# Kernel optimization log

Hardware: AMD Instinct MI355X
Metric: run time of the kernel (lower is better)

The kernel has to match this reference:

```python
import jax, jax.numpy as jnp
import numpy as np

B, L, V, A = 4096, 64, 50000, 1000
E, H, G, F2 = 32, 32, 256, 512


def _xavier(k, shape):
    fan_out, fan_in = shape
    a = np.sqrt(6.0 / (fan_in + fan_out)).astype(np.float32)
    return jax.random.uniform(k, shape, jnp.float32, -a, a)


def setup_inputs() -> dict:
    key = jax.random.key(0)
    ks = jax.random.split(key, 32)
    inp = {}
    inp["q"] = jax.random.randint(ks[0], (B, L), 0, V)
    for i in range(8):
        inp[f"sf{i}"] = jax.random.randint(ks[1 + i], (B, L), 0, V)
    inp["emb"] = _xavier(ks[9], (V, E))
    # torch LSTM weight layout: [4H, in] with gate order i,f,g,o; biases init to 0
    inp["q_Wih"] = _xavier(ks[10], (4 * H, E))
    inp["q_Whh"] = _xavier(ks[11], (4 * H, H))
    inp["q_b"] = jnp.zeros((4 * H,), jnp.float32)
    inp["sf_Wih"] = _xavier(ks[12], (4 * H, E))
    inp["sf_Whh"] = _xavier(ks[13], (4 * H, H))
    inp["sf_b"] = jnp.zeros((4 * H,), jnp.float32)
    inp["g1_W"] = _xavier(ks[14], (G, 2 * H + 1)); inp["g1_b"] = jnp.zeros((G,), jnp.float32)
    inp["g2_W"] = _xavier(ks[15], (G, G)); inp["g2_b"] = jnp.zeros((G,), jnp.float32)
    inp["g3_W"] = _xavier(ks[16], (G, G)); inp["g3_b"] = jnp.zeros((G,), jnp.float32)
    inp["g4_W"] = _xavier(ks[17], (G, G)); inp["g4_b"] = jnp.zeros((G,), jnp.float32)
    inp["f1_W"] = _xavier(ks[18], (G, G)); inp["f1_b"] = jnp.zeros((G,), jnp.float32)
    inp["f2_W"] = _xavier(ks[19], (F2, G)); inp["f2_b"] = jnp.zeros((F2,), jnp.float32)
    inp["f3_W"] = _xavier(ks[20], (A, F2)); inp["f3_b"] = jnp.zeros((A,), jnp.float32)
    return inp


def _lstm_last(x, Wih, Whh, b):
    """x: [L, N, E] -> final hidden state [N, H]. Torch gate order i,f,g,o."""
    n = x.shape[1]
    h_dim = Whh.shape[1]
    def step(carry, xt):
        h, c = carry
        gates = xt @ Wih.T + h @ Whh.T + b  # [N, 4H]
        i, f, g, o = jnp.split(gates, 4, axis=-1)
        c = jax.nn.sigmoid(f) * c + jax.nn.sigmoid(i) * jnp.tanh(g)
        h = jax.nn.sigmoid(o) * jnp.tanh(c)
        return (h, c), None
    init = (jnp.zeros((n, h_dim), x.dtype), jnp.zeros((n, h_dim), x.dtype))
    (h, _), _ = jax.lax.scan(step, init, x)
    return h


def _lin(x, W, b):
    return x @ W.T + b


def reference(q, sf0, sf1, sf2, sf3, sf4, sf5, sf6, sf7,
              emb, q_Wih, q_Whh, q_b, sf_Wih, sf_Whh, sf_b,
              g1_W, g1_b, g2_W, g2_b, g3_W, g3_b, g4_W, g4_b,
              f1_W, f1_b, f2_W, f2_b, f3_W, f3_b):
    # dropout in eval mode (identity)
    b, l = q.shape
    qe = emb[q].transpose(1, 0, 2)  # [L, B, E]
    hq = _lstm_last(qe, q_Wih, q_Whh, q_b)  # [B, H]

    sf = jnp.stack([sf0, sf1, sf2, sf3, sf4, sf5, sf6, sf7])  # [8, B, L]
    sfe = emb[sf]  # [8, B, L, E]
    sfe = sfe.transpose(2, 0, 1, 3).reshape(l, 8 * b, emb.shape[1])  # one fused LSTM over 8*B
    hs = _lstm_last(sfe, sf_Wih, sf_Whh, sf_b).reshape(8, b, -1)  # [8, B, H]

    pos = jnp.broadcast_to(jnp.arange(8, dtype=hs.dtype)[:, None, None], (8, b, 1))
    x = jnp.concatenate([hs, jnp.broadcast_to(hq, (8, b, hq.shape[-1])), pos], axis=-1)  # [8, B, 65]
    x = jax.nn.relu(_lin(x, g1_W, g1_b))
    x = jax.nn.relu(_lin(x, g2_W, g2_b))
    x = jax.nn.relu(_lin(x, g3_W, g3_b))
    x = jax.nn.relu(_lin(x, g4_W, g4_b))
    g_o = x.sum(axis=0)  # [B, 256] segment-sum over the 8 relations

    x = jax.nn.relu(_lin(g_o, f1_W, f1_b))
    x = jax.nn.relu(_lin(x, f2_W, f2_b))
    return _lin(x, f3_W, f3_b)  # [B, A]
```

## Files before the change

### kernel.cpp

```cpp
#include <hip/hip_runtime.h>
#include <stdint.h>
#include <stddef.h>

typedef __fp16 f16;
typedef __attribute__((ext_vector_type(8))) __fp16 half8;
typedef __attribute__((ext_vector_type(4))) __fp16 half4;
typedef __attribute__((ext_vector_type(4))) float f32x4;

static __device__ __forceinline__ f32x4 mfma16(half8 a, half8 b, f32x4 c) {
    return __builtin_amdgcn_mfma_f32_16x16x32_f16(a, b, c, 0, 0, 0);
}
static __device__ __forceinline__ float fexp2(float x) { float r; asm("v_exp_f32 %0, %1" : "=v"(r) : "v"(x)); return r; }
static __device__ __forceinline__ float frcp(float x)  { float r; asm("v_rcp_f32 %0, %1" : "=v"(r) : "v"(x)); return r; }

static constexpr float L2E  = 1.4426950408889634f;
static constexpr float L2E2 = 2.8853900817779268f;

static constexpr int LDA = 264;
static constexpr int LDF2 = 520;

static constexpr size_t OFF_EMB   = 0;
static constexpr size_t OFF_WQIH  = 3200000;
static constexpr size_t OFF_WQHH  = OFF_WQIH + 8192;
static constexpr size_t OFF_WSIH  = OFF_WQHH + 8192;
static constexpr size_t OFF_WSHH  = OFF_WSIH + 8192;
static constexpr size_t OFF_BQ    = OFF_WSHH + 8192;
static constexpr size_t OFF_BS    = OFF_BQ + 512;
static constexpr size_t OFF_G1WP  = OFF_BS + 512;
static constexpr size_t OFF_BIAS8 = OFF_G1WP + 32768;
static constexpr size_t OFF_G2W   = OFF_BIAS8 + 8192;
static constexpr size_t OFF_G3W   = OFF_G2W + 131072;
static constexpr size_t OFF_G4W   = OFF_G3W + 131072;
static constexpr size_t OFF_F1W   = OFF_G4W + 131072;
static constexpr size_t OFF_F2W   = OFF_F1W + 131072;
static constexpr size_t OFF_F3W   = OFF_F2W + 262144;
static constexpr size_t OFF_HS    = OFF_F3W + 1024000;
static constexpr size_t OFF_HQ    = OFF_HS + 2097152;
static constexpr size_t OFF_ACT2  = OFF_HQ + 262144;
static constexpr size_t WS_NEED   = OFF_ACT2 + 16777216;

struct CvtJobs { const float* src[7]; f16* dst[7]; int n[7]; };

__global__ __launch_bounds__(256) void cvt_prep(
    CvtJobs j,
    const float* __restrict__ g1W, const float* __restrict__ g1b,
    f16* __restrict__ wp, float* __restrict__ bias8,
    const float* __restrict__ qWih, const float* __restrict__ qWhh, const float* __restrict__ qb,
    const float* __restrict__ sWih, const float* __restrict__ sWhh, const float* __restrict__ sb,
    f16* __restrict__ wqih, f16* __restrict__ wqhh, float* __restrict__ bq,
    f16* __restrict__ wsih, f16* __restrict__ wshh, float* __restrict__ bs)
{
    int t = threadIdx.x;
    if (blockIdx.y < 7) {
        int jb = blockIdx.y;
        int i = (blockIdx.x * 256 + t) * 8;
        if (i >= j.n[jb]) return;
        const float* s = j.src[jb] + i;
        f32x4 a = *(const f32x4*)s;
        f32x4 b = *(const f32x4*)(s + 4);
        half8 o;
        o[0]=(f16)a[0]; o[1]=(f16)a[1]; o[2]=(f16)a[2]; o[3]=(f16)a[3];
        o[4]=(f16)b[0]; o[5]=(f16)b[1]; o[6]=(f16)b[2]; o[7]=(f16)b[3];
        *(half8*)(j.dst[jb] + i) = o;
        return;
    }
    if (blockIdx.x == 0) {
        int col = t;
        for (int k = 0; k < 64; k++) wp[col * 64 + k] = (f16)g1W[col * 65 + k];
        float wpos = g1W[col * 65 + 64];
        float b = g1b[col];
        for (int i = 0; i < 8; i++) bias8[i * 256 + col] = b + (float)i * wpos;
    } else if (blockIdx.x == 1) {
        for (int i = t; i < 4096; i += 256) {
            int row = i >> 5;
            float s = (row < 64 || row >= 96) ? -L2E : L2E2;
            wqih[i] = (f16)(qWih[i] * s);
            wqhh[i] = (f16)(qWhh[i] * s);
            wsih[i] = (f16)(sWih[i] * s);
            wshh[i] = (f16)(sWhh[i] * s);
        }
        if (t < 128) {
            float s = (t < 64 || t >= 96) ? -L2E : L2E2;
            bq[t] = qb[t] * s;
            bs[t] = sb[t] * s;
        }
    }
}

struct SfPtrs { const int* p[8]; };

__global__ __launch_bounds__(64) void lstm_kernel(
    SfPtrs sf, const int* __restrict__ qtok, const f16* __restrict__ emb_h,
    const f16* __restrict__ wih_sf, const f16* __restrict__ whh_sf, const float* __restrict__ b_sf,
    const f16* __restrict__ wih_q,  const f16* __restrict__ whh_q,  const float* __restrict__ b_q,
    f16* __restrict__ hs_out, f16* __restrict__ hq_out)
{
    __shared__ __align__(16) char hb0[16 * 80];
    __shared__ __align__(16) char hb1[16 * 80];
    int lane = threadIdx.x;
    int c15 = lane & 15, kq = lane >> 4;
    int sbase = blockIdx.x * 32;
    bool isq = sbase >= 32768;
    const f16* wih = isq ? wih_q : wih_sf;
    const f16* whh = isq ? whh_q : whh_sf;
    const float* bvec = isq ? b_q : b_sf;

    half8 wi[8], wh[8];
    f32x4 bc[8];
    #pragma unroll
    for (int n = 0; n < 8; n++) {
        wi[n] = *(const half8*)(wih + (n * 16 + c15) * 32 + kq * 8);
        wh[n] = *(const half8*)(whh + (n * 16 + c15) * 32 + kq * 8);
        bc[n] = *(const f32x4*)(bvec + n * 16 + kq * 4);
    }
    int sg0 = sbase + c15, sg1 = sbase + 16 + c15;
    const int* tp0; const int* tp1;
    if (isq) { tp0 = qtok + (sg0 - 32768) * 64; tp1 = qtok + (sg1 - 32768) * 64; }
    else     { tp0 = sf.p[sg0 >> 12] + (sg0 & 4095) * 64;
               tp1 = sf.p[sg1 >> 12] + (sg1 & 4095) * 64; }

    f32x4 zro = {0.f, 0.f, 0.f, 0.f};
    *(f32x4*)(hb0 + lane * 16) = zro;
    *(f32x4*)(hb1 + lane * 16) = zro;
    if (lane < 16) { *(f32x4*)(hb0 + 1024 + lane * 16) = zro;
                     *(f32x4*)(hb1 + 1024 + lane * 16) = zro; }

    float cst0[2][4] = {}, cst1[2][4] = {};
    const char* hrd0 = hb0 + c15 * 80 + kq * 16;
    const char* hrd1 = hb1 + c15 * 80 + kq * 16;

    half8 xf0 = *(const half8*)(emb_h + (size_t)tp0[0] * 32 + kq * 8);
    half8 xf1 = *(const half8*)(emb_h + (size_t)tp1[0] * 32 + kq * 8);

    #pragma unroll 1
    for (int t = 0; t < 64; t++) {
        half8 hf0 = *(const half8*)hrd0;
        half8 hf1 = *(const half8*)hrd1;
        f32x4 a0[8], a1[8];
        #pragma unroll
        for (int n = 0; n < 8; n++) a0[n] = mfma16(wi[n], xf0, bc[n]);
        #pragma unroll
        for (int n = 0; n < 8; n++) a1[n] = mfma16(wi[n], xf1, bc[n]);
        #pragma unroll
        for (int n = 0; n < 8; n++) a0[n] = mfma16(wh[n], hf0, a0[n]);
        #pragma unroll
        for (int n = 0; n < 8; n++) a1[n] = mfma16(wh[n], hf1, a1[n]);
        if (t < 63) {
            xf0 = *(const half8*)(emb_h + (size_t)tp0[t + 1] * 32 + kq * 8);
            xf1 = *(const half8*)(emb_h + (size_t)tp1[t + 1] * 32 + kq * 8);
        }
        #pragma unroll
        for (int jh = 0; jh < 2; jh++) {
            half4 hp;
            #pragma unroll
            for (int r = 0; r < 4; r++) {
                float ei = fexp2(a0[0 + jh][r]);
                float ef = fexp2(a0[2 + jh][r]);
                float eg = fexp2(a0[4 + jh][r]);
                float eo = fexp2(a0[6 + jh][r]);
                float t1 = 1.f + ei, t2 = 1.f + ef, t5 = 1.f + eo;
                float eg1 = eg + 1.f, egm = eg - 1.f;
                float num = fmaf(egm, t2, cst0[jh][r] * t1 * eg1);
                float cn  = num * frcp((t2 * t1) * eg1);
                cst0[jh][r] = cn;
                float ec  = fexp2(cn * L2E2);
                hp[r] = (f16)((ec - 1.f) * frcp((ec + 1.f) * t5));
            }
            *(half4*)(hb0 + c15 * 80 + jh * 32 + kq * 8) = hp;
        }
        #pragma unroll
        for (int jh = 0; jh < 2; jh++) {
            half4 hp;
            #pragma unroll
            for (int r = 0; r < 4; r++) {
                float ei = fexp2(a1[0 + jh][r]);
                float ef = fexp2(a1[2 + jh][r]);
                float eg = fexp2(a1[4 + jh][r]);
                float eo = fexp2(a1[6 + jh][r]);
                float t1 = 1.f + ei, t2 = 1.f + ef, t5 = 1.f + eo;
                float eg1 = eg + 1.f, egm = eg - 1.f;
                float num = fmaf(egm, t2, cst1[jh][r] * t1 * eg1);
                float cn  = num * frcp((t2 * t1) * eg1);
                cst1[jh][r] = cn;
                float ec  = fexp2(cn * L2E2);
                hp[r] = (f16)((ec - 1.f) * frcp((ec + 1.f) * t5));
            }
            *(half4*)(hb1 + c15 * 80 + jh * 32 + kq * 8) = hp;
        }
    }
    half8 hv0 = *(const half8*)hrd0;
    half8 hv1 = *(const half8*)hrd1;
    if (isq) {
        *(half8*)(hq_out + (size_t)(sg0 - 32768) * 32 + kq * 8) = hv0;
        *(half8*)(hq_out + (size_t)(sg1 - 32768) * 32 + kq * 8) = hv1;
    } else {
        *(half8*)(hs_out + (size_t)sg0 * 32 + kq * 8) = hv0;
        *(half8*)(hs_out + (size_t)sg1 * 32 + kq * 8) = hv1;
    }
}

template<bool TOGLOBAL>
static __device__ __forceinline__ void layer256(
    const f16 (* __restrict__ src)[LDA], f16 (* __restrict__ dst)[LDA],
    const f16* __restrict__ W, const float* __restrict__ bias,
    f16* __restrict__ gout, int m0, int wm, int wn, int c15, int kq)
{
    f32x4 acc[2][4];
    #pragma unroll
    for (int a = 0; a < 2; a++)
        #pragma unroll
        for (int b = 0; b < 4; b++) acc[a][b] = (f32x4){0.f, 0.f, 0.f, 0.f};
    #pragma unroll
    for (int k0 = 0; k0 < 8; k0++) {
        half8 av[2], bv[4];
        #pragma unroll
        for (int fm = 0; fm < 2; fm++) av[fm] = *(const half8*)(&src[wm * 32 + fm * 16 + c15][k0 * 32 + kq * 8]);
        #pragma unroll
        for (int fn = 0; fn < 4; fn++) bv[fn] = *(const half8*)(W + (size_t)(wn * 64 + fn * 16 + c15) * 256 + k0 * 32 + kq * 8);
        #pragma unroll
        for (int fm = 0; fm < 2; fm++)
            #pragma unroll
            for (int fn = 0; fn < 4; fn++) acc[fm][fn] = mfma16(av[fm], bv[fn], acc[fm][fn]);
    }
    #pragma unroll
    for (int fn = 0; fn < 4; fn++) {
        int col = wn * 64 + fn * 16 + c15;
        float bb = bias[col];
        #pragma unroll
        for (int fm = 0; fm < 2; fm++)
            #pragma unroll
            for (int r = 0; r < 4; r++) {
                float v = fmaxf(acc[fm][fn][r] + bb, 0.f);
                int row = wm * 32 + fm * 16 + kq * 4 + r;
                if (TOGLOBAL) gout[(size_t)(m0 + row) * 256 + col] = (f16)v;
                else          dst[row][col] = (f16)v;
            }
    }
}

__global__ __launch_bounds__(512) void gemm_g1234(
    const f16* __restrict__ hs, const f16* __restrict__ hq,
    const f16* __restrict__ g1wp, const float* __restrict__ bias8,
    const f16* __restrict__ g2w, const float* __restrict__ g2b,
    const f16* __restrict__ g3w, const float* __restrict__ g3b,
    const f16* __restrict__ g4w, const float* __restrict__ g4b,
    f16* __restrict__ act2)
{
    __shared__ __align__(16) f16 actA[64][LDA];
    __shared__ __align__(16) f16 actB[64][LDA];
    const int wv = threadIdx.x >> 6, lane = threadIdx.x & 63;
    const int c15 = lane & 15, kq = lane >> 4;
    const int wm = wv >> 2, wn = wv & 3;
    const int m0 = blockIdx.x * 64;
    const float* brow = bias8 + ((m0 >> 12) << 8);

    {
        f32x4 acc[2][4];
        #pragma unroll
        for (int a = 0; a < 2; a++)
            #pragma unroll
            for (int b = 0; b < 4; b++) acc[a][b] = (f32x4){0.f, 0.f, 0.f, 0.f};
        half8 av[2], bv[4];
        #pragma unroll
        for (int fm = 0; fm < 2; fm++) av[fm] = *(const half8*)(hs + (size_t)(m0 + wm * 32 + fm * 16 + c15) * 32 + kq * 8);
        #pragma unroll
        for (int fn = 0; fn < 4; fn++) bv[fn] = *(const half8*)(g1wp + (size_t)(wn * 64 + fn * 16 + c15) * 64 + kq * 8);
        #pragma unroll
        for (int fm = 0; fm < 2; fm++)
            #pragma unroll
            for (int fn = 0; fn < 4; fn++) acc[fm][fn] = mfma16(av[fm], bv[fn], acc[fm][fn]);
        #pragma unroll
        for (int fm = 0; fm < 2; fm++) av[fm] = *(const half8*)(hq + (size_t)((m0 + wm * 32 + fm * 16 + c15) & 4095) * 32 + kq * 8);
        #pragma unroll
        for (int fn = 0; fn < 4; fn++) bv[fn] = *(const half8*)(g1wp + (size_t)(wn * 64 + fn * 16 + c15) * 64 + 32 + kq * 8);
        #pragma unroll
        for (int fm = 0; fm < 2; fm++)
            #pragma unroll
            for (int fn = 0; fn < 4; fn++) acc[fm][fn] = mfma16(av[fm], bv[fn], acc[fm][fn]);
        #pragma unroll
        for (int fn = 0; fn < 4; fn++) {
            int col = wn * 64 + fn * 16 + c15;
            float bb = brow[col];
            #pragma unroll
            for (int fm = 0; fm < 2; fm++)
                #pragma unroll
                for (int r = 0; r < 4; r++)
                    actA[wm * 32 + fm * 16 + kq * 4 + r][col] = (f16)fmaxf(acc[fm][fn][r] + bb, 0.f);
        }
    }
    __syncthreads();
    layer256<false>(actA, actB, g2w, g2b, nullptr, m0, wm, wn, c15, kq);
    __syncthreads();
    layer256<false>(actB, actA, g3w, g3b, nullptr, m0, wm, wn, c15, kq);
    __syncthreads();
    layer256<true>(actA, actB, g4w, g4b, act2, m0, wm, wn, c15, kq);
}

__global__ __launch_bounds__(512) void f123s_kernel(
    const f16* __restrict__ act2,
    const f16* __restrict__ f1w, const float* __restrict__ f1b,
    const f16* __restrict__ f2w, const float* __restrict__ f2b,
    const f16* __restrict__ f3w, const float* __restrict__ f3b,
    float* __restrict__ out)
{
    __shared__ __align__(16) f16 smbuf[16][LDA];
    __shared__ __align__(16) f16 f1buf[16][LDA];
    __shared__ __align__(16) f16 f2buf[16][LDF2];
    const int b0 = blockIdx.x * 16;

    {
        int r = threadIdx.x >> 5, cb = (threadIdx.x & 31) * 8;
        float s[8] = {};
        #pragma unroll
        for (int i = 0; i < 8; i++) {
            half8 v = *(const half8*)(act2 + ((size_t)(i * 4096 + b0 + r)) * 256 + cb);
            #pragma unroll
            for (int q = 0; q < 8; q++) s[q] += (float)v[q];
        }
        half8 o;
        #pragma unroll
        for (int q = 0; q < 8; q++) o[q] = (f16)s[q];
        *(half8*)(&smbuf[r][cb]) = o;
    }
    __syncthreads();
    const int wv = threadIdx.x >> 6, lane = threadIdx.x & 63;
    const int c15 = lane & 15, kq = lane >> 4;

    {
        f32x4 acc[2];
        acc[0] = (f32x4){0.f, 0.f, 0.f, 0.f}; acc[1] = acc[0];
        #pragma unroll
        for (int k0 = 0; k0 < 8; k0++) {
            half8 a = *(const half8*)(&smbuf[c15][k0 * 32 + kq * 8]);
            #pragma unroll
            for (int fn = 0; fn < 2; fn++) {
                half8 bv = *(const half8*)(f1w + (size_t)(wv * 32 + fn * 16 + c15) * 256 + k0 * 32 + kq * 8);
                acc[fn] = mfma16(a, bv, acc[fn]);
            }
        }
        #pragma unroll
        for (int fn = 0; fn < 2; fn++) {
            int col = wv * 32 + fn * 16 + c15;
            float bb = f1b[col];
            #pragma unroll
            for (int r = 0; r < 4; r++)
                f1buf[kq * 4 + r][col] = (f16)fmaxf(acc[fn][r] + bb, 0.f);
        }
    }
    __syncthreads();
    {
        f32x4 acc[4];
        #pragma unroll
        for (int b = 0; b < 4; b++) acc[b] = (f32x4){0.f, 0.f, 0.f, 0.f};
        #pragma unroll
        for (int k0 = 0; k0 < 8; k0++) {
            half8 a = *(const half8*)(&f1buf[c15][k0 * 32 + kq * 8]);
            #pragma unroll
            for (int fn = 0; fn < 4; fn++) {
                half8 bv = *(const half8*)(f2w + (size_t)(wv * 64 + fn * 16 + c15) * 256 + k0 * 32 + kq * 8);
                acc[fn] = mfma16(a, bv, acc[fn]);
            }
        }
        #pragma unroll
        for (int fn = 0; fn < 4; fn++) {
            int col = wv * 64 + fn * 16 + c15;
            float bb = f2b[col];
            #pragma unroll
            for (int r = 0; r < 4; r++)
                f2buf[kq * 4 + r][col] = (f16)fmaxf(acc[fn][r] + bb, 0.f);
        }
    }
    __syncthreads();
    {
        f32x4 acc[8];
        #pragma unroll
        for (int b = 0; b < 8; b++) acc[b] = (f32x4){0.f, 0.f, 0.f, 0.f};
        #pragma unroll
        for (int k0 = 0; k0 < 16; k0++) {
            half8 a = *(const half8*)(&f2buf[c15][k0 * 32 + kq * 8]);
            #pragma unroll
            for (int fn = 0; fn < 8; fn++) {
                int col = wv * 128 + fn * 16 + c15;
                int cl = col < 1000 ? col : 999;
                half8 bv = *(const half8*)(f3w + (size_t)cl * 512 + k0 * 32 + kq * 8);
                acc[fn] = mfma16(a, bv, acc[fn]);
            }
        }
        #pragma unroll
        for (int fn = 0; fn < 8; fn++) {
            int col = wv * 128 + fn * 16 + c15;
            if (col < 1000) {
                float bb = f3b[col];
                #pragma unroll
                for (int r = 0; r < 4; r++)
                    out[(size_t)(b0 + kq * 4 + r) * 1000 + col] = acc[fn][r] + bb;
            }
        }
    }
}

extern "C" void kernel_launch(void* const* d_in, const int* in_sizes, int n_in,
                              void* d_out, int out_size, void* d_ws, size_t ws_size,
                              hipStream_t stream)
{
    if (ws_size < WS_NEED) return;
    const int* q_tok = (const int*)d_in[0];
    SfPtrs sf;
    for (int i = 0; i < 8; i++) sf.p[i] = (const int*)d_in[1 + i];
    const float* emb_f = (const float*)d_in[9];
    const float* qWih = (const float*)d_in[10];
    const float* qWhh = (const float*)d_in[11];
    const float* q_b  = (const float*)d_in[12];
    const float* sWih = (const float*)d_in[13];
    const float* sWhh = (const float*)d_in[14];
    const float* s_b  = (const float*)d_in[15];
    const float* g1W  = (const float*)d_in[16];
    const float* g1b  = (const float*)d_in[17];
    const float* g2W  = (const float*)d_in[18];
    const float* g2b  = (const float*)d_in[19];
    const float* g3W  = (const float*)d_in[20];
    const float* g3b  = (const float*)d_in[21];
    const float* g4W  = (const float*)d_in[22];
    const float* g4b  = (const float*)d_in[23];
    const float* f1W  = (const float*)d_in[24];
    const float* f1b  = (const float*)d_in[25];
    const float* f2W  = (const float*)d_in[26];
    const float* f2b  = (const float*)d_in[27];
    const float* f3W  = (const float*)d_in[28];
    const float* f3b  = (const float*)d_in[29];

    char* ws = (char*)d_ws;
    f16* emb_h = (f16*)(ws + OFF_EMB);
    f16* wqih  = (f16*)(ws + OFF_WQIH);
    f16* wqhh  = (f16*)(ws + OFF_WQHH);
    f16* wsih  = (f16*)(ws + OFF_WSIH);
    f16* wshh  = (f16*)(ws + OFF_WSHH);
    float* bq  = (float*)(ws + OFF_BQ);
    float* bs  = (float*)(ws + OFF_BS);
    f16* g1wp  = (f16*)(ws + OFF_G1WP);
    float* bias8 = (float*)(ws + OFF_BIAS8);
    f16* g2w = (f16*)(ws + OFF_G2W);
    f16* g3w = (f16*)(ws + OFF_G3W);
    f16* g4w = (f16*)(ws + OFF_G4W);
    f16* f1w = (f16*)(ws + OFF_F1W);
    f16* f2w = (f16*)(ws + OFF_F2W);
    f16* f3w = (f16*)(ws + OFF_F3W);
    f16* hs  = (f16*)(ws + OFF_HS);
    f16* hq  = (f16*)(ws + OFF_HQ);
    f16* act2 = (f16*)(ws + OFF_ACT2);

    CvtJobs cj;
    const float* srcs[7] = {emb_f, g2W, g3W, g4W, f1W, f2W, f3W};
    f16* dsts[7]         = {emb_h, g2w, g3w, g4w, f1w, f2w, f3w};
    int ns[7] = {1600000, 65536, 65536, 65536, 65536, 131072, 512000};
    for (int i = 0; i < 7; i++) { cj.src[i] = srcs[i]; cj.dst[i] = dsts[i]; cj.n[i] = ns[i]; }

    cvt_prep<<<dim3(782, 8), 256, 0, stream>>>(cj, g1W, g1b, g1wp, bias8,
                                               qWih, qWhh, q_b, sWih, sWhh, s_b,
                                               wqih, wqhh, bq, wsih, wshh, bs);
    lstm_kernel<<<1152, 64, 0, stream>>>(sf, q_tok, emb_h, wsih, wshh, bs, wqih, wqhh, bq, hs, hq);
    gemm_g1234<<<512, 512, 0, stream>>>(hs, hq, g1wp, bias8, g2w, g2b, g3w, g3b, g4w, g4b, act2);
    f123s_kernel<<<256, 512, 0, stream>>>(act2, f1w, f1b, f2w, f2b, f3w, f3b, (float*)d_out);
}
```

Before: 394.1 us.

## Exchange LSTM hidden state via ds_bpermute and halve sequences per wave

The LSTM kernel now handles 16 sequences per 64-lane block instead of 32, doubling the grid. It drops the shared-memory round trip for the hidden state and instead rebuilds the MFMA B-operand fragment directly from the gate outputs using eight ds_bpermute lane shuffles per step. The aim is to shorten the serial per-step dependency chain (LDS write, then read) and to raise occupancy with more, lighter waves. In exchange, each wave no longer interleaves two independent recurrences to hide MFMA and transcendental latency.

```diff
diff --git a/kernel.cpp b/kernel.cpp
--- a/kernel.cpp
+++ b/kernel.cpp
@@ -6,6 +6,9 @@
 typedef __attribute__((ext_vector_type(8))) __fp16 half8;
 typedef __attribute__((ext_vector_type(4))) __fp16 half4;
 typedef __attribute__((ext_vector_type(4))) float f32x4;
+typedef unsigned int u32;
+typedef __attribute__((ext_vector_type(2))) u32 u32x2;
+typedef __attribute__((ext_vector_type(4))) u32 u32x4;
 
 static __device__ __forceinline__ f32x4 mfma16(half8 a, half8 b, f32x4 c) {
     return __builtin_amdgcn_mfma_f32_16x16x32_f16(a, b, c, 0, 0, 0);
@@ -95,11 +98,9 @@
     const f16* __restrict__ wih_q,  const f16* __restrict__ whh_q,  const float* __restrict__ b_q,
     f16* __restrict__ hs_out, f16* __restrict__ hq_out)
 {
-    __shared__ __align__(16) char hb0[16 * 80];
-    __shared__ __align__(16) char hb1[16 * 80];
     int lane = threadIdx.x;
     int c15 = lane & 15, kq = lane >> 4;
-    int sbase = blockIdx.x * 32;
+    int sbase = blockIdx.x * 16;
     bool isq = sbase >= 32768;
     const f16* wih = isq ? wih_q : wih_sf;
     const f16* whh = isq ? whh_q : whh_sf;
@@ -113,90 +114,69 @@
         wh[n] = *(const half8*)(whh + (n * 16 + c15) * 32 + kq * 8);
         bc[n] = *(const f32x4*)(bvec + n * 16 + kq * 4);
     }
-    int sg0 = sbase + c15, sg1 = sbase + 16 + c15;
-    const int* tp0; const int* tp1;
-    if (isq) { tp0 = qtok + (sg0 - 32768) * 64; tp1 = qtok + (sg1 - 32768) * 64; }
-    else     { tp0 = sf.p[sg0 >> 12] + (sg0 & 4095) * 64;
-               tp1 = sf.p[sg1 >> 12] + (sg1 & 4095) * 64; }
-
-    f32x4 zro = {0.f, 0.f, 0.f, 0.f};
-    *(f32x4*)(hb0 + lane * 16) = zro;
-    *(f32x4*)(hb1 + lane * 16) = zro;
-    if (lane < 16) { *(f32x4*)(hb0 + 1024 + lane * 16) = zro;
-                     *(f32x4*)(hb1 + 1024 + lane * 16) = zro; }
-
-    float cst0[2][4] = {}, cst1[2][4] = {};
-    const char* hrd0 = hb0 + c15 * 80 + kq * 16;
-    const char* hrd1 = hb1 + c15 * 80 + kq * 16;
-
-    half8 xf0 = *(const half8*)(emb_h + (size_t)tp0[0] * 32 + kq * 8);
-    half8 xf1 = *(const half8*)(emb_h + (size_t)tp1[0] * 32 + kq * 8);
+    int sg = sbase + c15;
+    const int* tp;
+    if (isq) tp = qtok + (sg - 32768) * 64;
+    else     tp = sf.p[sg >> 12] + (sg & 4095) * 64;
+
+    int i1 = (c15 + ((kq & 1) << 5)) << 2;
+    int i2 = i1 + 64;
+    bool hi = kq >= 2;
+
+    float cst[2][4] = {};
+    half8 hf = {};
+    half8 xf = *(const half8*)(emb_h + (size_t)tp[0] * 32 + kq * 8);
 
     #pragma unroll 1
     for (int t = 0; t < 64; t++) {
-        half8 hf0 = *(const half8*)hrd0;
-        half8 hf1 = *(const half8*)hrd1;
-        f32x4 a0[8], a1[8];
-        #pragma unroll
-        for (int n = 0; n < 8; n++) a0[n] = mfma16(wi[n], xf0, bc[n]);
-        #pragma unroll
-        for (int n = 0; n < 8; n++) a1[n] = mfma16(wi[n], xf1, bc[n]);
-        #pragma unroll
-        for (int n = 0; n < 8; n++) a0[n] = mfma16(wh[n], hf0, a0[n]);
-        #pragma unroll
-        for (int n = 0; n < 8; n++) a1[n] = mfma16(wh[n], hf1, a1[n]);
+        f32x4 acc[8];
+        #pragma unroll
+        for (int n = 0; n < 8; n++) acc[n] = mfma16(wi[n], xf, bc[n]);
+        #pragma unroll
+        for (int n = 0; n < 8; n++) acc[n] = mfma16(wh[n], hf, acc[n]);
         if (t < 63) {
-            xf0 = *(const half8*)(emb_h + (size_t)tp0[t + 1] * 32 + kq * 8);
-            xf1 = *(const half8*)(emb_h + (size_t)tp1[t + 1] * 32 + kq * 8);
-        }
+            int tk = tp[t + 1];
+            xf = *(const half8*)(emb_h + (size_t)tk * 32 + kq * 8);
+        }
+        half4 hp0, hp1;
         #pragma unroll
         for (int jh = 0; jh < 2; jh++) {
-            half4 hp;
             #pragma unroll
             for (int r = 0; r < 4; r++) {
-                float ei = fexp2(a0[0 + jh][r]);
-                float ef = fexp2(a0[2 + jh][r]);
-                float eg = fexp2(a0[4 + jh][r]);
-                float eo = fexp2(a0[6 + jh][r]);
+                float ei = fexp2(acc[0 + jh][r]);
+                float ef = fexp2(acc[2 + jh][r]);
+                float eg = fexp2(acc[4 + jh][r]);
+                float eo = fexp2(acc[6 + jh][r]);
                 float t1 = 1.f + ei, t2 = 1.f + ef, t5 = 1.f + eo;
                 float eg1 = eg + 1.f, egm = eg - 1.f;
-                float num = fmaf(egm, t2, cst0[jh][r] * t1 * eg1);
-                float cn  = num * frcp((t2 * t1) * eg1);
-                cst0[jh][r] = cn;
+                float t1e = t1 * eg1;
+                float num = fmaf(egm, t2, cst[jh][r] * t1e);
+                float cn  = num * frcp(t1e * t2);
+                cst[jh][r] = cn;
                 float ec  = fexp2(cn * L2E2);
-                hp[r] = (f16)((ec - 1.f) * frcp((ec + 1.f) * t5));
-            }
-            *(half4*)(hb0 + c15 * 80 + jh * 32 + kq * 8) = hp;
-        }
-        #pragma unroll
-        for (int jh = 0; jh < 2; jh++) {
-            half4 hp;
-            #pragma unroll
-            for (int r = 0; r < 4; r++) {
-                float ei = fexp2(a1[0 + jh][r]);
-                float ef = fexp2(a1[2 + jh][r]);
-                float eg = fexp2(a1[4 + jh][r]);
-                float eo = fexp2(a1[6 + jh][r]);
-                float t1 = 1.f + ei, t2 = 1.f + ef, t5 = 1.f + eo;
-                float eg1 = eg + 1.f, egm = eg - 1.f;
-                float num = fmaf(egm, t2, cst1[jh][r] * t1 * eg1);
-                float cn  = num * frcp((t2 * t1) * eg1);
-                cst1[jh][r] = cn;
-                float ec  = fexp2(cn * L2E2);
-                hp[r] = (f16)((ec - 1.f) * frcp((ec + 1.f) * t5));
-            }
-            *(half4*)(hb1 + c15 * 80 + jh * 32 + kq * 8) = hp;
-        }
-    }
-    half8 hv0 = *(const half8*)hrd0;
-    half8 hv1 = *(const half8*)hrd1;
-    if (isq) {
-        *(half8*)(hq_out + (size_t)(sg0 - 32768) * 32 + kq * 8) = hv0;
-        *(half8*)(hq_out + (size_t)(sg1 - 32768) * 32 + kq * 8) = hv1;
-    } else {
-        *(half8*)(hs_out + (size_t)sg0 * 32 + kq * 8) = hv0;
-        *(half8*)(hs_out + (size_t)sg1 * 32 + kq * 8) = hv1;
-    }
+                float hv  = (ec - 1.f) * frcp((ec + 1.f) * t5);
+                if (jh == 0) hp0[r] = (f16)hv; else hp1[r] = (f16)hv;
+            }
+        }
+        u32x2 pa = __builtin_bit_cast(u32x2, hp0);
+        u32x2 pb = __builtin_bit_cast(u32x2, hp1);
+        int ra0 = __builtin_amdgcn_ds_bpermute(i1, (int)pa.x);
+        int ra1 = __builtin_amdgcn_ds_bpermute(i1, (int)pa.y);
+        int rb0 = __builtin_amdgcn_ds_bpermute(i1, (int)pb.x);
+        int rb1 = __builtin_amdgcn_ds_bpermute(i1, (int)pb.y);
+        int ra2 = __builtin_amdgcn_ds_bpermute(i2, (int)pa.x);
+        int ra3 = __builtin_amdgcn_ds_bpermute(i2, (int)pa.y);
+        int rb2 = __builtin_amdgcn_ds_bpermute(i2, (int)pb.x);
+        int rb3 = __builtin_amdgcn_ds_bpermute(i2, (int)pb.y);
+        u32x4 w;
+        w.x = (u32)(hi ? rb0 : ra0);
+        w.y = (u32)(hi ? rb1 : ra1);
+        w.z = (u32)(hi ? rb2 : ra2);
+        w.w = (u32)(hi ? rb3 : ra3);
+        hf = __builtin_bit_cast(half8, w);
+    }
+    if (isq) *(half8*)(hq_out + (size_t)(sg - 32768) * 32 + kq * 8) = hf;
+    else     *(half8*)(hs_out + (size_t)sg * 32 + kq * 8) = hf;
 }
 
 template<bool TOGLOBAL>
@@ -458,7 +438,7 @@
     cvt_prep<<<dim3(782, 8), 256, 0, stream>>>(cj, g1W, g1b, g1wp, bias8,
                                                qWih, qWhh, q_b, sWih, sWhh, s_b,
                                                wqih, wqhh, bq, wsih, wshh, bs);
-    lstm_kernel<<<1152, 64, 0, stream>>>(sf, q_tok, emb_h, wsih, wshh, bs, wqih, wqhh, bq, hs, hq);
+    lstm_kernel<<<2304, 64, 0, stream>>>(sf, q_tok, emb_h, wsih, wshh, bs, wqih, wqhh, bq, hs, hq);
     gemm_g1234<<<512, 512, 0, stream>>>(hs, hq, g1wp, bias8, g2w, g2b, g3w, g3b, g4w, g4b, act2);
     f123s_kernel<<<256, 512, 0, stream>>>(act2, f1w, f1b, f2w, f2b, f3w, f3b, (float*)d_out);
 }
```

New measurement: 344.2 us. -12.7%, faster.
